# Optimization experiments

Measured on AMD Instinct MI355X. Metric: run time of the kernel, lower is better.

The kernel has to match this reference:

```python
import jax, jax.numpy as jnp
import numpy as np

N, D, NUM_CLASSES = 4096, 1024, 64


def setup_inputs() -> dict:
    key = jax.random.key(0)
    k1, k2 = jax.random.split(key)
    inputs = jax.random.normal(k1, (N, D), dtype=jnp.float32)
    labels = jax.random.randint(k2, (N,), 0, NUM_CLASSES, dtype=jnp.int64)
    return {"inputs": inputs, "labels": labels}


def reference(inputs, labels):
    # dist_mat = inputs @ inputs.T  (raw dot-product 'cosine_dist', no normalization)
    dist = jnp.matmul(inputs, inputs.T)  # [N, N]
    n = inputs.shape[0]
    same = labels[:, None] == labels[None, :]          # [N, N]
    eye = jnp.eye(n, dtype=bool)
    is_pos = same & ~eye                               # same label, excluding self
    is_neg = ~same                                     # different label
    # hardest-positive: +2 penalty on non-positive entries, then row argmin
    d_ap = jnp.where(is_pos, dist, dist + 2.0)
    # 'easiest' negative: +2 penalty on non-negative entries, then row argmin
    d_an = jnp.where(is_neg, dist, dist + 2.0)
    id_ap = jnp.argmin(d_ap, axis=1)                   # [N]
    id_an = jnp.argmin(d_an, axis=1)                   # [N]
    # (The original also computes a semi-hard id_an_semi, but returns id_an;
    #  that block is dead code w.r.t. the output, so it is omitted.)
    return (inputs[id_ap], inputs[id_an])
```

## Files before the change

### kernel.cpp

```cpp
#include <hip/hip_runtime.h>
#include <cstdint>

#define N 4096
#define D 1024
#define KC_COUNT (D / 32)
#define NP 4128
#define RGP (NP / 16)
#define TG (NP / 96)
#define NBLK (TG * (TG + 1) / 2)

typedef _Float16 f16;
typedef __attribute__((ext_vector_type(4))) _Float16 f16x4;
typedef __attribute__((ext_vector_type(8))) _Float16 f16x8;
typedef __attribute__((ext_vector_type(4))) float f32x4;

__device__ __forceinline__ unsigned int orderable(float f) {
    unsigned int b = __float_as_uint(f);
    return (b & 0x80000000u) ? ~b : (b | 0x80000000u);
}

__device__ __forceinline__ void async_copy16(const f16* g, f16* l) {
    __builtin_amdgcn_global_load_lds(
        (const __attribute__((address_space(1))) uint32_t*)(const void*)g,
        (__attribute__((address_space(3))) uint32_t*)(void*)l,
        16 , 0 , 0 );
}

#define KSPAN 256
#define SS_STRIDE (KSPAN + 24)
__global__ __launch_bounds__(256) void split_swizzle(
    const float* __restrict__ X, f16* __restrict__ Xsw,
    unsigned long long* __restrict__ keys)
{
    __shared__ f16 Hs[16 * SS_STRIDE];
    __shared__ f16 Ls[16 * SS_STRIDE];
    const int tid = threadIdx.x;
    const int bid = blockIdx.x;
    const int rg = bid >> 2, kq = bid & 3;
    if (bid < 32) keys[bid * 256 + tid] = 0xFFFFFFFFFFFFFFFFull;

    if (rg >= 256) {
        const uint4 z = {0, 0, 0, 0};
#pragma unroll
        for (int i = 0; i < 4; ++i) {
            const int o = i * 256 + tid;
            const int kcl = o >> 7, rem = o & 127;
            const int kc = kq * 8 + kcl;
            *(uint4*)(Xsw + (((size_t)rg * KC_COUNT + kc) * 2) * 512 + rem * 8) = z;
        }
        return;
    }

#pragma unroll
    for (int i = 0; i < 4; ++i) {
        const int idx4 = i * 256 + tid;
        const int row = idx4 >> 6, c4 = idx4 & 63;
        const float4 v = *(const float4*)(X + (size_t)(rg * 16 + row) * D + kq * KSPAN + c4 * 4);
        const float xs[4] = {v.x, v.y, v.z, v.w};
        f16x4 h, l;
#pragma unroll
        for (int e = 0; e < 4; ++e) {
            f16 hh = (f16)xs[e];
            h[e] = hh;
            l[e] = (f16)(xs[e] - (float)hh);
        }
        *(f16x4*)(Hs + row * SS_STRIDE + c4 * 4) = h;
        *(f16x4*)(Ls + row * SS_STRIDE + c4 * 4) = l;
    }
    __syncthreads();

#pragma unroll
    for (int hl = 0; hl < 2; ++hl) {
        const f16* lds = hl ? Ls : Hs;
#pragma unroll
        for (int i = 0; i < 2; ++i) {
            const int o = i * 256 + tid;
            const int kcl = o >> 6, lo_ = o & 63;
            const int q = lo_ >> 4, m = lo_ & 15;
            const uint4 v = *(const uint4*)(lds + m * SS_STRIDE + kcl * 32 + q * 8);
            const int kc = kq * 8 + kcl;
            *(uint4*)(Xsw + (((size_t)rg * KC_COUNT + kc) * 2 + hl) * 512 + lo_ * 8) = v;
        }
    }
}

__global__ __launch_bounds__(256, 4) void gemm_argmin_sym(
    const f16* __restrict__ Xsw, const int* __restrict__ labels,
    unsigned long long* __restrict__ keys_ap,
    unsigned long long* __restrict__ keys_an)
{
    __shared__ f16 As[6 * 2 * 512];
    __shared__ f16 Bs[6 * 2 * 512];

    int r = blockIdx.x, ti = 0;
    while (r >= TG - ti) { r -= TG - ti; ++ti; }
    const int tj = ti + r;

    const int tid = threadIdx.x;
    const int lane = tid & 63;
    const int w = tid >> 6;
    const int wr = w >> 1, wc = w & 1;
    const int rowBase = ti * 96, colBase = tj * 96;

    f32x4 acc[3][3];
#pragma unroll
    for (int mi = 0; mi < 3; ++mi)
#pragma unroll
        for (int ni = 0; ni < 3; ++ni) acc[mi][ni] = (f32x4){0.f, 0.f, 0.f, 0.f};

    const f16* g[6];
    f16* lp[6];
#pragma unroll
    for (int j = 0; j < 6; ++j) {
        int c = w * 6 + j;
        int isB = c >= 12, rem = isB ? c - 12 : c, rgL = rem >> 1, hl = rem & 1;
        int rgG = (isB ? tj : ti) * 6 + rgL;
        g[j] = Xsw + ((((size_t)rgG * KC_COUNT) * 2 + hl) * 64 + lane) * 8;
        lp[j] = (isB ? Bs : As) + (rgL * 2 + hl) * 512;
    }

    for (int kc = 0; kc < KC_COUNT; ++kc) {
#pragma unroll
        for (int j = 0; j < 6; ++j)
            async_copy16(g[j] + (size_t)kc * 1024, lp[j]);
        __syncthreads();

        f16x8 ah[3], al[3], bh[3], bl[3];
#pragma unroll
        for (int t2 = 0; t2 < 3; ++t2) {
            int rgA = wr * 3 + t2, rgB = wc * 3 + t2;
            ah[t2] = *(const f16x8*)(As + (rgA * 2 + 0) * 512 + lane * 8);
            al[t2] = *(const f16x8*)(As + (rgA * 2 + 1) * 512 + lane * 8);
            bh[t2] = *(const f16x8*)(Bs + (rgB * 2 + 0) * 512 + lane * 8);
            bl[t2] = *(const f16x8*)(Bs + (rgB * 2 + 1) * 512 + lane * 8);
        }
#pragma unroll
        for (int mi = 0; mi < 3; ++mi)
#pragma unroll
            for (int ni = 0; ni < 3; ++ni) {
                acc[mi][ni] = __builtin_amdgcn_mfma_f32_16x16x32_f16(
                    ah[mi], bh[ni], acc[mi][ni], 0, 0, 0);
                acc[mi][ni] = __builtin_amdgcn_mfma_f32_16x16x32_f16(
                    ah[mi], bl[ni], acc[mi][ni], 0, 0, 0);
                acc[mi][ni] = __builtin_amdgcn_mfma_f32_16x16x32_f16(
                    al[mi], bh[ni], acc[mi][ni], 0, 0, 0);
            }
        __syncthreads();
    }

    const int g16 = lane >> 4, c16 = lane & 15;

    int ljv[3], liv[3][4];
#pragma unroll
    for (int ni = 0; ni < 3; ++ni) {
        const int j = colBase + wc * 48 + ni * 16 + c16;
        ljv[ni] = (j < N) ? labels[j] : -1;
    }
#pragma unroll
    for (int mi = 0; mi < 3; ++mi)
#pragma unroll
        for (int reg = 0; reg < 4; ++reg) {
            const int i = rowBase + wr * 48 + mi * 16 + g16 * 4 + reg;
            liv[mi][reg] = (i < N) ? labels[i] : -1;
        }

#pragma unroll
    for (int mi = 0; mi < 3; ++mi) {
#pragma unroll
        for (int reg = 0; reg < 4; ++reg) {
            const int i = rowBase + wr * 48 + mi * 16 + g16 * 4 + reg;
            const int li = liv[mi][reg];
            float bestAp = __builtin_huge_valf(); int jAp = 0;
            float bestAn = __builtin_huge_valf(); int jAn = 0;
#pragma unroll
            for (int ni = 0; ni < 3; ++ni) {
                const int jcol = colBase + wc * 48 + ni * 16 + c16;
                const float v = acc[mi][ni][reg];
                const bool same = (li == ljv[ni]);
                const float vap = (same && (i != jcol)) ? v : v + 2.0f;
                const float van = (!same) ? v : v + 2.0f;
                if (vap < bestAp) { bestAp = vap; jAp = jcol; }
                if (van < bestAn) { bestAn = van; jAn = jcol; }
            }
            unsigned long long kap =
                ((unsigned long long)orderable(bestAp) << 32) | (unsigned)jAp;
            unsigned long long kan =
                ((unsigned long long)orderable(bestAn) << 32) | (unsigned)jAn;
#pragma unroll
            for (int off = 1; off < 16; off <<= 1) {
                unsigned long long o = __shfl_xor(kap, off); kap = o < kap ? o : kap;
                o = __shfl_xor(kan, off); kan = o < kan ? o : kan;
            }
            if (c16 == 0 && i < N) {
                atomicMin(&keys_ap[i], kap);
                atomicMin(&keys_an[i], kan);
            }
        }
    }

    if (ti != tj) {
#pragma unroll
        for (int ni = 0; ni < 3; ++ni) {
            const int j = colBase + wc * 48 + ni * 16 + c16;
            const int lj = ljv[ni];
            float bestAp = __builtin_huge_valf(); int iAp = 0;
            float bestAn = __builtin_huge_valf(); int iAn = 0;
#pragma unroll
            for (int mi = 0; mi < 3; ++mi)
#pragma unroll
                for (int reg = 0; reg < 4; ++reg) {
                    const int i = rowBase + wr * 48 + mi * 16 + g16 * 4 + reg;
                    const float v = acc[mi][ni][reg];
                    const bool same = (liv[mi][reg] == lj);
                    const float vap = same ? v : v + 2.0f;
                    const float van = (!same) ? v : v + 2.0f;
                    if (vap < bestAp) { bestAp = vap; iAp = i; }
                    if (van < bestAn) { bestAn = van; iAn = i; }
                }
            unsigned long long kap =
                ((unsigned long long)orderable(bestAp) << 32) | (unsigned)iAp;
            unsigned long long kan =
                ((unsigned long long)orderable(bestAn) << 32) | (unsigned)iAn;
#pragma unroll
            for (int off = 16; off < 64; off <<= 1) {
                unsigned long long o = __shfl_xor(kap, off); kap = o < kap ? o : kap;
                o = __shfl_xor(kan, off); kan = o < kan ? o : kan;
            }
            if (g16 == 0 && j < N) {
                atomicMin(&keys_ap[j], kap);
                atomicMin(&keys_an[j], kan);
            }
        }
    }
}

__global__ void gather_rows(const float* __restrict__ A,
                            const unsigned long long* __restrict__ keys_ap,
                            const unsigned long long* __restrict__ keys_an,
                            float* __restrict__ out)
{
    const int row = blockIdx.x;
    const int t = threadIdx.x;
    const int ja = (int)(keys_ap[row] & 0xFFFFFFFFull);
    const int jn = (int)(keys_an[row] & 0xFFFFFFFFull);
    const float4* Av = (const float4*)A;
    float4* Ov = (float4*)out;
    Ov[(size_t)row * (D / 4) + t]       = Av[(size_t)ja * (D / 4) + t];
    Ov[(size_t)(N + row) * (D / 4) + t] = Av[(size_t)jn * (D / 4) + t];
}

extern "C" void kernel_launch(void* const* d_in, const int* in_sizes, int n_in,
                              void* d_out, int out_size, void* d_ws, size_t ws_size,
                              hipStream_t stream) {
    const float* A = (const float*)d_in[0];
    const int* labels = (const int*)d_in[1];
    float* out = (float*)d_out;

    unsigned long long* keys = (unsigned long long*)d_ws;
    f16* Xsw = (f16*)((char*)d_ws + 65536);

    split_swizzle<<<RGP * 4, 256, 0, stream>>>(A, Xsw, keys);
    gemm_argmin_sym<<<NBLK, 256, 0, stream>>>(Xsw, labels, keys, keys + N);
    gather_rows<<<N, 256, 0, stream>>>(A, keys, keys + N, out);
}
```

Baseline: 155.2 us.

## Switch symmetric GEMM to 128x128 tiles with 8 waves, dropping row padding

The symmetric distance GEMM moves from 96x96 tiles with 4 waves to 128x128 tiles with 8 waves, each wave computing 64x32. Because 4096 divides evenly by 128, the padded row count and its zero-fill path, bounds checks and masked label loads are all removed. Larger tiles raise arithmetic intensity per LDS load and cut the number of blocks and atomics. The cost is fewer blocks (528 instead of 946), which may leave CUs less evenly loaded, plus more threads per block sharing each barrier.

```diff
diff --git a/kernel.cpp b/kernel.cpp
--- a/kernel.cpp
+++ b/kernel.cpp
@@ -4,10 +4,8 @@
 #define N 4096
 #define D 1024
 #define KC_COUNT (D / 32)
-#define NP 4128
-#define RGP (NP / 16)
-#define TG (NP / 96)
-#define NBLK (TG * (TG + 1) / 2)
+#define TB (N / 128)
+#define NBLK (TB * (TB + 1) / 2)
 
 typedef _Float16 f16;
 typedef __attribute__((ext_vector_type(4))) _Float16 f16x4;
@@ -39,18 +37,6 @@
     const int rg = bid >> 2, kq = bid & 3;
     if (bid < 32) keys[bid * 256 + tid] = 0xFFFFFFFFFFFFFFFFull;
 
-    if (rg >= 256) {
-        const uint4 z = {0, 0, 0, 0};
-#pragma unroll
-        for (int i = 0; i < 4; ++i) {
-            const int o = i * 256 + tid;
-            const int kcl = o >> 7, rem = o & 127;
-            const int kc = kq * 8 + kcl;
-            *(uint4*)(Xsw + (((size_t)rg * KC_COUNT + kc) * 2) * 512 + rem * 8) = z;
-        }
-        return;
-    }
-
 #pragma unroll
     for (int i = 0; i < 4; ++i) {
         const int idx4 = i * 256 + tid;
@@ -84,60 +70,64 @@
     }
 }
 
-__global__ __launch_bounds__(256, 4) void gemm_argmin_sym(
+__global__ __launch_bounds__(512, 4) void gemm_argmin_sym(
     const f16* __restrict__ Xsw, const int* __restrict__ labels,
     unsigned long long* __restrict__ keys_ap,
     unsigned long long* __restrict__ keys_an)
 {
-    __shared__ f16 As[6 * 2 * 512];
-    __shared__ f16 Bs[6 * 2 * 512];
+    __shared__ f16 As[8 * 2 * 512];
+    __shared__ f16 Bs[8 * 2 * 512];
 
     int r = blockIdx.x, ti = 0;
-    while (r >= TG - ti) { r -= TG - ti; ++ti; }
+    while (r >= TB - ti) { r -= TB - ti; ++ti; }
     const int tj = ti + r;
 
     const int tid = threadIdx.x;
     const int lane = tid & 63;
     const int w = tid >> 6;
-    const int wr = w >> 1, wc = w & 1;
-    const int rowBase = ti * 96, colBase = tj * 96;
-
-    f32x4 acc[3][3];
-#pragma unroll
-    for (int mi = 0; mi < 3; ++mi)
-#pragma unroll
-        for (int ni = 0; ni < 3; ++ni) acc[mi][ni] = (f32x4){0.f, 0.f, 0.f, 0.f};
-
-    const f16* g[6];
-    f16* lp[6];
-#pragma unroll
-    for (int j = 0; j < 6; ++j) {
-        int c = w * 6 + j;
-        int isB = c >= 12, rem = isB ? c - 12 : c, rgL = rem >> 1, hl = rem & 1;
-        int rgG = (isB ? tj : ti) * 6 + rgL;
+    const int wr = w >> 2, wc = w & 3;
+    const int rowBase = ti * 128, colBase = tj * 128;
+
+    f32x4 acc[4][2];
+#pragma unroll
+    for (int mi = 0; mi < 4; ++mi)
+#pragma unroll
+        for (int ni = 0; ni < 2; ++ni) acc[mi][ni] = (f32x4){0.f, 0.f, 0.f, 0.f};
+
+    const f16* g[4];
+    f16* lp[4];
+#pragma unroll
+    for (int j = 0; j < 4; ++j) {
+        int c = w * 4 + j;
+        int isB = c >> 4, rem = c & 15, rgL = rem >> 1, hl = rem & 1;
+        int rgG = (isB ? tj : ti) * 8 + rgL;
         g[j] = Xsw + ((((size_t)rgG * KC_COUNT) * 2 + hl) * 64 + lane) * 8;
         lp[j] = (isB ? Bs : As) + (rgL * 2 + hl) * 512;
     }
 
     for (int kc = 0; kc < KC_COUNT; ++kc) {
 #pragma unroll
-        for (int j = 0; j < 6; ++j)
+        for (int j = 0; j < 4; ++j)
             async_copy16(g[j] + (size_t)kc * 1024, lp[j]);
         __syncthreads();
 
-        f16x8 ah[3], al[3], bh[3], bl[3];
-#pragma unroll
-        for (int t2 = 0; t2 < 3; ++t2) {
-            int rgA = wr * 3 + t2, rgB = wc * 3 + t2;
+        f16x8 ah[4], al[4], bh[2], bl[2];
+#pragma unroll
+        for (int t2 = 0; t2 < 4; ++t2) {
+            int rgA = wr * 4 + t2;
             ah[t2] = *(const f16x8*)(As + (rgA * 2 + 0) * 512 + lane * 8);
             al[t2] = *(const f16x8*)(As + (rgA * 2 + 1) * 512 + lane * 8);
+        }
+#pragma unroll
+        for (int t2 = 0; t2 < 2; ++t2) {
+            int rgB = wc * 2 + t2;
             bh[t2] = *(const f16x8*)(Bs + (rgB * 2 + 0) * 512 + lane * 8);
             bl[t2] = *(const f16x8*)(Bs + (rgB * 2 + 1) * 512 + lane * 8);
         }
 #pragma unroll
-        for (int mi = 0; mi < 3; ++mi)
-#pragma unroll
-            for (int ni = 0; ni < 3; ++ni) {
+        for (int mi = 0; mi < 4; ++mi)
+#pragma unroll
+            for (int ni = 0; ni < 2; ++ni) {
                 acc[mi][ni] = __builtin_amdgcn_mfma_f32_16x16x32_f16(
                     ah[mi], bh[ni], acc[mi][ni], 0, 0, 0);
                 acc[mi][ni] = __builtin_amdgcn_mfma_f32_16x16x32_f16(
@@ -150,31 +140,27 @@
 
     const int g16 = lane >> 4, c16 = lane & 15;
 
-    int ljv[3], liv[3][4];
-#pragma unroll
-    for (int ni = 0; ni < 3; ++ni) {
-        const int j = colBase + wc * 48 + ni * 16 + c16;
-        ljv[ni] = (j < N) ? labels[j] : -1;
-    }
-#pragma unroll
-    for (int mi = 0; mi < 3; ++mi)
+    int ljv[2], liv[4][4];
+#pragma unroll
+    for (int ni = 0; ni < 2; ++ni)
+        ljv[ni] = labels[colBase + wc * 32 + ni * 16 + c16];
+#pragma unroll
+    for (int mi = 0; mi < 4; ++mi)
+#pragma unroll
+        for (int reg = 0; reg < 4; ++reg)
+            liv[mi][reg] = labels[rowBase + wr * 64 + mi * 16 + g16 * 4 + reg];
+
+#pragma unroll
+    for (int mi = 0; mi < 4; ++mi) {
 #pragma unroll
         for (int reg = 0; reg < 4; ++reg) {
-            const int i = rowBase + wr * 48 + mi * 16 + g16 * 4 + reg;
-            liv[mi][reg] = (i < N) ? labels[i] : -1;
-        }
-
-#pragma unroll
-    for (int mi = 0; mi < 3; ++mi) {
-#pragma unroll
-        for (int reg = 0; reg < 4; ++reg) {
-            const int i = rowBase + wr * 48 + mi * 16 + g16 * 4 + reg;
+            const int i = rowBase + wr * 64 + mi * 16 + g16 * 4 + reg;
             const int li = liv[mi][reg];
             float bestAp = __builtin_huge_valf(); int jAp = 0;
             float bestAn = __builtin_huge_valf(); int jAn = 0;
 #pragma unroll
-            for (int ni = 0; ni < 3; ++ni) {
-                const int jcol = colBase + wc * 48 + ni * 16 + c16;
+            for (int ni = 0; ni < 2; ++ni) {
+                const int jcol = colBase + wc * 32 + ni * 16 + c16;
                 const float v = acc[mi][ni][reg];
                 const bool same = (li == ljv[ni]);
                 const float vap = (same && (i != jcol)) ? v : v + 2.0f;
@@ -191,7 +177,7 @@
                 unsigned long long o = __shfl_xor(kap, off); kap = o < kap ? o : kap;
                 o = __shfl_xor(kan, off); kan = o < kan ? o : kan;
             }
-            if (c16 == 0 && i < N) {
+            if (c16 == 0) {
                 atomicMin(&keys_ap[i], kap);
                 atomicMin(&keys_an[i], kan);
             }
@@ -200,16 +186,16 @@
 
     if (ti != tj) {
 #pragma unroll
-        for (int ni = 0; ni < 3; ++ni) {
-            const int j = colBase + wc * 48 + ni * 16 + c16;
+        for (int ni = 0; ni < 2; ++ni) {
+            const int j = colBase + wc * 32 + ni * 16 + c16;
             const int lj = ljv[ni];
             float bestAp = __builtin_huge_valf(); int iAp = 0;
             float bestAn = __builtin_huge_valf(); int iAn = 0;
 #pragma unroll
-            for (int mi = 0; mi < 3; ++mi)
+            for (int mi = 0; mi < 4; ++mi)
 #pragma unroll
                 for (int reg = 0; reg < 4; ++reg) {
-                    const int i = rowBase + wr * 48 + mi * 16 + g16 * 4 + reg;
+                    const int i = rowBase + wr * 64 + mi * 16 + g16 * 4 + reg;
                     const float v = acc[mi][ni][reg];
                     const bool same = (liv[mi][reg] == lj);
                     const float vap = same ? v : v + 2.0f;
@@ -226,7 +212,7 @@
                 unsigned long long o = __shfl_xor(kap, off); kap = o < kap ? o : kap;
                 o = __shfl_xor(kan, off); kan = o < kan ? o : kan;
             }
-            if (g16 == 0 && j < N) {
+            if (g16 == 0) {
                 atomicMin(&keys_ap[j], kap);
                 atomicMin(&keys_an[j], kan);
             }
@@ -259,7 +245,7 @@
     unsigned long long* keys = (unsigned long long*)d_ws;
     f16* Xsw = (f16*)((char*)d_ws + 65536);
 
-    split_swizzle<<<RGP * 4, 256, 0, stream>>>(A, Xsw, keys);
-    gemm_argmin_sym<<<NBLK, 256, 0, stream>>>(Xsw, labels, keys, keys + N);
+    split_swizzle<<<(N / 16) * 4, 256, 0, stream>>>(A, Xsw, keys);
+    gemm_argmin_sym<<<NBLK, 512, 0, stream>>>(Xsw, labels, keys, keys + N);
     gather_rows<<<N, 256, 0, stream>>>(A, keys, keys + N, out);
 }
```

New measurement: 175.8 us. 13.3% more time.
